# Optimization experiments

Measured on AMD Instinct MI355X. Metric: run time of the kernel, lower is better.

## Reference

```python
import jax, jax.numpy as jnp
import numpy as np

B, N, T, D = 4, 128, 64, 768
L_ATTN, HEADS = 4, 8
M_SSM = 4
D_INNER, D_STATE, HEADDIM = 1536, 64, 64
NHEADS = D_INNER // HEADDIM  # 24
D_CONV = 4
CONV_DIM = D_INNER + 2 * D_STATE  # 1664
IN_PROJ = 2 * D_INNER + 2 * D_STATE + NHEADS  # 3224
FFN_MULT = 4


def rmsnorm(x, w, eps=1e-5):
    return x * jax.lax.rsqrt(jnp.mean(x * x, -1, keepdims=True) + eps) * w


def mha(q_in, kv_in, Wq, Wk, Wv, Wo):
    b, lq, d = q_in.shape
    lk = kv_in.shape[1]
    dh = d // HEADS
    scale = 1.0 / float(np.sqrt(dh))
    q = (q_in @ Wq).reshape(b, lq, HEADS, dh)
    k = (kv_in @ Wk).reshape(b, lk, HEADS, dh)
    v = (kv_in @ Wv).reshape(b, lk, HEADS, dh)
    scores = jnp.einsum('bqhd,bkhd->bhqk', q, k) * scale
    attn = jax.nn.softmax(scores, axis=-1)
    o = jnp.einsum('bhqk,bkhd->bqhd', attn, v).reshape(b, lq, d)
    return o @ Wo


def mamba_block(x, in_proj_w, conv_w, conv_b, dt_bias, A_log, D_skip, norm_w, out_proj_w):
    # x: (b, l, D); selective-scan (Mamba2) with scalar-per-head A, ngroups=1
    b, l, _ = x.shape
    zxbcdt = x @ in_proj_w                       # (b, l, IN_PROJ)
    z = zxbcdt[..., :D_INNER]
    xBC = zxbcdt[..., D_INNER:D_INNER + CONV_DIM]
    dt = zxbcdt[..., D_INNER + CONV_DIM:]        # (b, l, NHEADS)
    # causal depthwise conv1d, kernel D_CONV
    xp = jnp.pad(xBC, ((0, 0), (D_CONV - 1, 0), (0, 0)))
    xc = sum(conv_w[k] * xp[:, k:k + l] for k in range(D_CONV)) + conv_b
    xc = jax.nn.silu(xc)
    xs = xc[..., :D_INNER].reshape(b, l, NHEADS, HEADDIM)
    Bm = xc[..., D_INNER:D_INNER + D_STATE]      # (b, l, D_STATE)
    Cm = xc[..., D_INNER + D_STATE:]             # (b, l, D_STATE)
    dt = jax.nn.softplus(dt + dt_bias)           # (b, l, NHEADS)
    A = -jnp.exp(A_log)                          # (NHEADS,)
    h0 = jnp.zeros((b, NHEADS, HEADDIM, D_STATE), x.dtype)

    def step(h, inp):
        xt, Bt, Ct, dtt = inp                    # (b,nh,hd), (b,ds), (b,ds), (b,nh)
        dA = jnp.exp(dtt * A)                    # (b, nh)
        h = h * dA[:, :, None, None] + (dtt[:, :, None, None] * xt[..., None]) * Bt[:, None, None, :]
        y = jnp.einsum('bhps,bs->bhp', h, Ct)
        return h, y

    hT, ys = jax.lax.scan(step, h0, (xs.transpose(1, 0, 2, 3), Bm.transpose(1, 0, 2), Cm.transpose(1, 0, 2), dt.transpose(1, 0, 2)))
    y = ys.transpose(1, 0, 2, 3) + D_skip[:, None] * xs  # skip connection per head
    y = y.reshape(b, l, D_INNER)
    y = rmsnorm(y * jax.nn.silu(z), norm_w)      # gated RMSNorm
    return y @ out_proj_w, hT


def reference(precepts, actions, attn_norm1_w, Wq, Wk, Wv, Wo, attn_norm2_w, ffn_w1, ffn_b1, ffn_w2, ffn_b2, ssm_norm_w, in_proj_w, conv_w, conv_b, dt_bias, A_log, D_skip, mamba_norm_w, out_proj_w, proj_w, proj_b):
    p = precepts.reshape(B * N, T, D)
    a = actions.reshape(B * N, T, D)
    for i in range(L_ATTN):
        cross = (i + 1) % 2 == 0
        q = rmsnorm(p, attn_norm1_w[i])
        kv = a if cross else q
        p = p + mha(q, kv, Wq[i], Wk[i], Wv[i], Wo[i])
        h_ = rmsnorm(p, attn_norm2_w[i])
        p = p + (jax.nn.gelu(h_ @ ffn_w1[i] + ffn_b1[i]) @ ffn_w2[i] + ffn_b2[i])
    # (b n) t d -> (b t) n d : scan over the num_steps axis
    z = p.reshape(B, N, T, D).transpose(0, 2, 1, 3).reshape(B * T, N, D)
    h_last = None
    for m in range(M_SSM):
        out, h_last = mamba_block(rmsnorm(z, ssm_norm_w[m]), in_proj_w[m], conv_w[m], conv_b[m], dt_bias[m], A_log[m], D_skip[m], mamba_norm_w[m], out_proj_w[m])
        z = z + out
    y = z @ proj_w + proj_b
    y = y.reshape(B, T, N, D).transpose(0, 2, 1, 3)  # b n t d
    return y, h_last


def setup_inputs() -> dict:
    key = jax.random.key(0)
    ks = jax.random.split(key, 16)
    s = 0.02
    f32 = jnp.float32
    return {
        'precepts': jax.random.normal(ks[0], (B, N, T, D), f32),
        'actions': jax.random.normal(ks[1], (B, N, T, D), f32),
        'attn_norm1_w': jnp.ones((L_ATTN, D), f32),
        'Wq': s * jax.random.normal(ks[2], (L_ATTN, D, D), f32),
        'Wk': s * jax.random.normal(ks[3], (L_ATTN, D, D), f32),
        'Wv': s * jax.random.normal(ks[4], (L_ATTN, D, D), f32),
        'Wo': s * jax.random.normal(ks[5], (L_ATTN, D, D), f32),
        'attn_norm2_w': jnp.ones((L_ATTN, D), f32),
        'ffn_w1': s * jax.random.normal(ks[6], (L_ATTN, D, FFN_MULT * D), f32),
        'ffn_b1': jnp.zeros((L_ATTN, FFN_MULT * D), f32),
        'ffn_w2': s * jax.random.normal(ks[7], (L_ATTN, FFN_MULT * D, D), f32),
        'ffn_b2': jnp.zeros((L_ATTN, D), f32),
        'ssm_norm_w': jnp.ones((M_SSM, D), f32),
        'in_proj_w': s * jax.random.normal(ks[8], (M_SSM, D, IN_PROJ), f32),
        'conv_w': s * jax.random.normal(ks[9], (M_SSM, D_CONV, CONV_DIM), f32),
        'conv_b': jnp.zeros((M_SSM, CONV_DIM), f32),
        'dt_bias': jax.random.uniform(ks[10], (M_SSM, NHEADS), f32, -2.0, 0.0),
        'A_log': jnp.broadcast_to(jnp.log(jnp.arange(1, NHEADS + 1, dtype=f32)), (M_SSM, NHEADS)),
        'D_skip': jnp.ones((M_SSM, NHEADS), f32),
        'mamba_norm_w': jnp.ones((M_SSM, D_INNER), f32),
        'out_proj_w': s * jax.random.normal(ks[11], (M_SSM, D_INNER, D), f32),
        'proj_w': s * jax.random.normal(ks[12], (D, D), f32),
        'proj_b': jnp.zeros((D,), f32),
    }
```

## Files before the change

kernel.cpp:

```cpp
#include <hip/hip_runtime.h>
#include <hip/hip_bf16.h>
#include <math.h>

constexpr long TOK  = 32768;
constexpr long HALF = TOK * 768;
constexpr int FLAG_ACC = 1, FLAG_GELU = 2, FLAG_PERM = 4, FLAG_BF16 = 8;

typedef __bf16 bf16x8 __attribute__((ext_vector_type(8)));
typedef __bf16 bf16x4 __attribute__((ext_vector_type(4)));
typedef float  f32x4  __attribute__((ext_vector_type(4)));

__device__ __forceinline__ void gload_lds16(const void* g, void* l) {
    __builtin_amdgcn_global_load_lds(
        (const __attribute__((address_space(1))) void*)g,
        (__attribute__((address_space(3))) void*)l, 16, 0, 0);
}
__device__ __forceinline__ float bf2f(__hip_bfloat16 v) { return __bfloat162float(v); }

__global__ __launch_bounds__(512, 2) void gemm256(
    const __hip_bfloat16* __restrict__ A,
    const __hip_bfloat16* __restrict__ BT,
    const float* __restrict__ bias,
    void* __restrict__ Cv, int ldc,
    int M, int N, int K, int flags, int moff)
{
    __shared__ __align__(16) __hip_bfloat16 As[2][256 * 64];
    __shared__ __align__(16) __hip_bfloat16 Bs[2][256 * 64];
    const int tid = threadIdx.x;
    const int wid = tid >> 6, lane = tid & 63;
    const int wm = wid >> 2, wn = wid & 3;
    const int lrow = lane & 15, lk = lane >> 4;
    const int nwg = gridDim.x * gridDim.y;
    const int orig = blockIdx.y * gridDim.x + blockIdx.x;
    const int q8 = nwg >> 3, r8 = nwg & 7;
    const int xcd = orig & 7, off = orig >> 3;
    const int wgid = (xcd < r8 ? xcd * (q8 + 1) : r8 * (q8 + 1) + (xcd - r8) * q8) + off;
    const int bm = (wgid / gridDim.x) * 256, bn = (wgid % gridDim.x) * 256;
    const int nk = K >> 6;

    f32x4 acc[4][8];
#pragma unroll
    for (int nf = 0; nf < 4; nf++)
#pragma unroll
        for (int mf = 0; mf < 8; mf++) acc[nf][mf] = f32x4{0.f, 0.f, 0.f, 0.f};

    bf16x8 Af[4][2];
    bf16x8 B0[2][2];
    bf16x8 B1[2][2];

    auto stage = [&](int kt, int which) {
        if (kt >= nk) return;
        const int dbuf = kt & 1;
        __hip_bfloat16* lbase = (which >= 2 ? &Bs[dbuf][0] : &As[dbuf][0]) + (which & 1) * 8192;
        const __hip_bfloat16* g = (which >= 2 ? BT : A);
        const int trow = (which >= 2 ? bn : bm) + (which & 1) * 128;
#pragma unroll
        for (int i = 0; i < 2; i++) {
            const int slot = i * 512 + tid;
            const int rl = slot >> 3, ch = slot & 7;
            const int sc = (ch ^ (rl & 7)) * 8;
            const long src = (long)(trow + rl) * K + (long)kt * 64 + sc;
            char* l = (char*)lbase + (i * 512 + wid * 64) * 16;
            gload_lds16(g + src, l);
        }
    };
    auto readA = [&](int dbuf, int mh) {
#pragma unroll
        for (int mq = 0; mq < 4; mq++)
#pragma unroll
            for (int ks = 0; ks < 2; ks++) {
                const int r = wm * 128 + mh * 64 + mq * 16 + lrow;
                const int ch = ((ks * 4 + lk) ^ (r & 7)) * 8;
                Af[mq][ks] = *(const bf16x8*)(const void*)&As[dbuf][r * 64 + ch];
            }
    };
    auto readB0 = [&](int dbuf) {
#pragma unroll
        for (int nf = 0; nf < 2; nf++)
#pragma unroll
            for (int ks = 0; ks < 2; ks++) {
                const int r = wn * 64 + nf * 16 + lrow;
                const int ch = ((ks * 4 + lk) ^ (r & 7)) * 8;
                B0[nf][ks] = *(const bf16x8*)(const void*)&Bs[dbuf][r * 64 + ch];
            }
    };
    auto readB1 = [&](int dbuf) {
#pragma unroll
        for (int nf = 0; nf < 2; nf++)
#pragma unroll
            for (int ks = 0; ks < 2; ks++) {
                const int r = wn * 64 + (2 + nf) * 16 + lrow;
                const int ch = ((ks * 4 + lk) ^ (r & 7)) * 8;
                B1[nf][ks] = *(const bf16x8*)(const void*)&Bs[dbuf][r * 64 + ch];
            }
    };

    stage(0, 0); stage(0, 1); stage(0, 2); stage(0, 3);
    stage(1, 2); stage(1, 3);
    asm volatile("s_waitcnt vmcnt(4)" ::: "memory");
    __builtin_amdgcn_s_barrier();

    for (int kt = 0; kt < nk; kt++) {
        const int cur = kt & 1;
        readA(cur, 0); readB0(cur);
        stage(kt + 1, 0); stage(kt + 1, 1);
        __builtin_amdgcn_s_barrier();
        __builtin_amdgcn_s_setprio(1);
#pragma unroll
        for (int ks = 0; ks < 2; ks++)
#pragma unroll
            for (int nf = 0; nf < 2; nf++)
#pragma unroll
                for (int mq = 0; mq < 4; mq++)
                    acc[nf][mq] = __builtin_amdgcn_mfma_f32_16x16x32_bf16(B0[nf][ks], Af[mq][ks], acc[nf][mq], 0, 0, 0);
        __builtin_amdgcn_s_setprio(0);
        __builtin_amdgcn_s_barrier();
        readB1(cur);
        __builtin_amdgcn_s_barrier();
        __builtin_amdgcn_s_setprio(1);
#pragma unroll
        for (int ks = 0; ks < 2; ks++)
#pragma unroll
            for (int nf = 0; nf < 2; nf++)
#pragma unroll
                for (int mq = 0; mq < 4; mq++)
                    acc[2 + nf][mq] = __builtin_amdgcn_mfma_f32_16x16x32_bf16(B1[nf][ks], Af[mq][ks], acc[2 + nf][mq], 0, 0, 0);
        __builtin_amdgcn_s_setprio(0);
        __builtin_amdgcn_s_barrier();
        readA(cur, 1);
        stage(kt + 2, 2);
        __builtin_amdgcn_s_barrier();
        __builtin_amdgcn_s_setprio(1);
#pragma unroll
        for (int ks = 0; ks < 2; ks++)
#pragma unroll
            for (int nf = 0; nf < 2; nf++)
#pragma unroll
                for (int mq = 0; mq < 4; mq++)
                    acc[2 + nf][4 + mq] = __builtin_amdgcn_mfma_f32_16x16x32_bf16(B1[nf][ks], Af[mq][ks], acc[2 + nf][4 + mq], 0, 0, 0);
        __builtin_amdgcn_s_setprio(0);
        __builtin_amdgcn_s_barrier();
        stage(kt + 2, 3);
        if (kt + 2 < nk) asm volatile("s_waitcnt vmcnt(4)" ::: "memory");
        else             asm volatile("s_waitcnt vmcnt(0)" ::: "memory");
        __builtin_amdgcn_s_barrier();
        __builtin_amdgcn_s_setprio(1);
#pragma unroll
        for (int ks = 0; ks < 2; ks++)
#pragma unroll
            for (int nf = 0; nf < 2; nf++)
#pragma unroll
                for (int mq = 0; mq < 4; mq++)
                    acc[nf][4 + mq] = __builtin_amdgcn_mfma_f32_16x16x32_bf16(B0[nf][ks], Af[mq][ks], acc[nf][4 + mq], 0, 0, 0);
        __builtin_amdgcn_s_setprio(0);
        __builtin_amdgcn_s_barrier();
    }

    float* Cf = (float*)Cv;
    __hip_bfloat16* Cb = (__hip_bfloat16*)Cv;
    if (flags & FLAG_BF16) {
        char* lw = (char*)&As[0][0] + (size_t)wid * (64 * 176);
        const int colg = bn + wn * 64;
#pragma unroll
        for (int half = 0; half < 2; half++) {
#pragma unroll
            for (int nf = 0; nf < 4; nf++) {
                const int col = nf * 16 + lk * 4;
                f32x4 b4 = f32x4{0.f, 0.f, 0.f, 0.f};
                if (bias) b4 = *(const f32x4*)&bias[colg + col];
#pragma unroll
                for (int m4 = 0; m4 < 4; m4++) {
                    const int row = m4 * 16 + lrow;
                    f32x4 v = acc[nf][half * 4 + m4] + b4;
                    if (flags & FLAG_GELU) {
#pragma unroll
                        for (int j = 0; j < 4; j++) {
                            const float x = v[j];
                            const float u = 1.5957691216057308f * (x + 0.044715f * x * x * x);
                            v[j] = x / (1.f + __expf(-u));
                        }
                    }
                    bf16x4 o;
                    o[0] = (__bf16)v[0]; o[1] = (__bf16)v[1];
                    o[2] = (__bf16)v[2]; o[3] = (__bf16)v[3];
                    *(bf16x4*)(void*)(lw + row * 176 + col * 2) = o;
                }
            }
            asm volatile("s_waitcnt lgkmcnt(0)" ::: "memory");
#pragma unroll
            for (int rr = 0; rr < 8; rr++) {
                const int row = rr * 8 + (lane >> 3);
                const long gr = (long)(bm + wm * 128 + half * 64 + row);
                const bf16x8 d = *(const bf16x8*)(const void*)(lw + row * 176 + (lane & 7) * 16);
                *(bf16x8*)(void*)&Cb[gr * ldc + colg + (lane & 7) * 8] = d;
            }
            asm volatile("s_waitcnt lgkmcnt(0)" ::: "memory");
        }
    } else {
#pragma unroll
        for (int nf = 0; nf < 4; nf++) {
            const int gcb = bn + wn * 64 + nf * 16 + lk * 4;
            if (gcb >= N) continue;
            f32x4 b4 = f32x4{0.f, 0.f, 0.f, 0.f};
            if (bias) b4 = *(const f32x4*)&bias[gcb];
#pragma unroll
            for (int mf = 0; mf < 8; mf++) {
                const int gr = bm + wm * 128 + mf * 16 + lrow;
                f32x4 v = acc[nf][mf] + b4;
                if (flags & FLAG_GELU) {
#pragma unroll
                    for (int j = 0; j < 4; j++) {
                        const float x = v[j];
                        const float u = 1.5957691216057308f * (x + 0.044715f * x * x * x);
                        v[j] = x / (1.f + __expf(-u));
                    }
                }
                if (flags & FLAG_PERM) {
                    const int mg = moff + gr;
                    const int b_ = mg >> 13, t_ = (mg >> 7) & 63, n_ = mg & 127;
                    *(f32x4*)&Cf[(((long)(b_ * 128 + n_)) * 64 + t_) * ldc + gcb] = v;
                } else if (flags & FLAG_ACC) {
                    float* dst = &Cf[(long)gr * ldc + gcb];
                    f32x4 old = *(const f32x4*)dst;
                    *(f32x4*)dst = old + v;
                } else {
                    *(f32x4*)&Cf[(long)gr * ldc + gcb] = v;
                }
            }
        }
    }
}

__global__ __launch_bounds__(256) void gemm_bf16(
    const __hip_bfloat16* __restrict__ A,
    const __hip_bfloat16* __restrict__ BT,
    const float* __restrict__ bias,
    void* __restrict__ Cv, int ldc,
    int M, int N, int K, int flags, int moff)
{
    __shared__ __hip_bfloat16 As[2][128 * 32];
    __shared__ __hip_bfloat16 Bs[2][128 * 32];
    const int tid = threadIdx.x;
    const int wv = tid >> 6, lane = tid & 63;
    const int nwg = gridDim.x * gridDim.y;
    const int orig = blockIdx.y * gridDim.x + blockIdx.x;
    const int q8 = nwg >> 3, r8 = nwg & 7;
    const int xcd = orig & 7, off = orig >> 3;
    const int wgid = (xcd < r8 ? xcd * (q8 + 1) : r8 * (q8 + 1) + (xcd - r8) * q8) + off;
    const int bm = (wgid / gridDim.x) * 128, bn = (wgid % gridDim.x) * 128;
    const int wr = (wv >> 1) * 64, wc = (wv & 1) * 64;
    const int lrow = lane & 15, lk = lane >> 4;
    const int ck = (lk ^ (lrow & 3) ^ ((lrow >> 2) & 3)) * 8;

    f32x4 acc[4][4];
#pragma unroll
    for (int n = 0; n < 4; n++)
#pragma unroll
        for (int m = 0; m < 4; m++) acc[n][m] = f32x4{0.f, 0.f, 0.f, 0.f};

    const int nk = K >> 5;
    auto stage = [&](int kt, int buf) {
#pragma unroll
        for (int i = 0; i < 2; i++) {
            const int lin = i * 256 + tid;
            const int row = lin >> 2;
            const int ks  = (((lin & 3) ^ (row & 3) ^ ((row >> 2) & 3)) * 8);
            const long asrc = (long)(bm + row) * K + kt * 32 + ks;
            const long bsrc = (long)(bn + row) * K + kt * 32 + ks;
            char* la = (char*)&As[buf][0] + (i * 256 + wv * 64) * 16;
            char* lb = (char*)&Bs[buf][0] + (i * 256 + wv * 64) * 16;
            gload_lds16(A + asrc, la);
            gload_lds16(BT + bsrc, lb);
        }
    };

    stage(0, 0);
    __syncthreads();
    for (int kt = 0; kt < nk; kt++) {
        const int cur = kt & 1;
        if (kt + 1 < nk) stage(kt + 1, cur ^ 1);
        bf16x8 af[4], bfr[4];
#pragma unroll
        for (int m = 0; m < 4; m++) {
            af[m]  = *(const bf16x8*)(const void*)&As[cur][(wr + m * 16 + lrow) * 32 + ck];
            bfr[m] = *(const bf16x8*)(const void*)&Bs[cur][(wc + m * 16 + lrow) * 32 + ck];
        }
#pragma unroll
        for (int n = 0; n < 4; n++)
#pragma unroll
            for (int m = 0; m < 4; m++)
                acc[n][m] = __builtin_amdgcn_mfma_f32_16x16x32_bf16(bfr[n], af[m], acc[n][m], 0, 0, 0);
        __syncthreads();
    }

    float* Cf = (float*)Cv;
    __hip_bfloat16* Cb = (__hip_bfloat16*)Cv;
#pragma unroll
    for (int n = 0; n < 4; n++) {
        const int gcb = bn + wc + n * 16 + lk * 4;
        if (gcb >= N) continue;
        f32x4 b4 = f32x4{0.f, 0.f, 0.f, 0.f};
        if (bias) b4 = *(const f32x4*)&bias[gcb];
#pragma unroll
        for (int m = 0; m < 4; m++) {
            const int gr = bm + wr + m * 16 + lrow;
            f32x4 v = acc[n][m] + b4;
            if (flags & FLAG_GELU) {
#pragma unroll
                for (int j = 0; j < 4; j++) {
                    const float x = v[j];
                    const float u = 1.5957691216057308f * (x + 0.044715f * x * x * x);
                    v[j] = x / (1.f + __expf(-u));
                }
            }
            if (flags & FLAG_PERM) {
                const int mg = moff + gr;
                const int b_ = mg >> 13, t_ = (mg >> 7) & 63, n_ = mg & 127;
                *(f32x4*)&Cf[(((long)(b_ * 128 + n_)) * 64 + t_) * ldc + gcb] = v;
            } else if (flags & FLAG_BF16) {
                __hip_bfloat16 o0 = __float2bfloat16(v[0]), o1 = __float2bfloat16(v[1]);
                __hip_bfloat16 o2 = __float2bfloat16(v[2]), o3 = __float2bfloat16(v[3]);
                ushort4 o = { *(ushort*)&o0, *(ushort*)&o1, *(ushort*)&o2, *(ushort*)&o3 };
                *(ushort4*)&Cb[(long)gr * ldc + gcb] = o;
            } else if (flags & FLAG_ACC) {
                float* dst = &Cf[(long)gr * ldc + gcb];
                f32x4 old = *(const f32x4*)dst;
                *(f32x4*)dst = old + v;
            } else {
                *(f32x4*)&Cf[(long)gr * ldc + gcb] = v;
            }
        }
    }
}

__global__ void convT_kernel(const float* __restrict__ W, __hip_bfloat16* __restrict__ WT,
                             int K, int N, int Npad)
{
    __shared__ float t[32][33];
    const int k0 = blockIdx.y * 32, n0 = blockIdx.x * 32;
    const int tx = threadIdx.x & 31, ty = threadIdx.x >> 5;
#pragma unroll
    for (int i = 0; i < 4; i++) {
        int k = k0 + ty + i * 8, n = n0 + tx;
        t[ty + i * 8][tx] = (k < K && n < N) ? W[(long)k * N + n] : 0.f;
    }
    __syncthreads();
#pragma unroll
    for (int i = 0; i < 4; i++) {
        int n = n0 + ty + i * 8, k = k0 + tx;
        if (n < Npad && k < K) WT[(long)n * K + k] = __float2bfloat16(t[tx][ty + i * 8]);
    }
}

__global__ void cvt_kernel(const float4* __restrict__ x, ushort4* __restrict__ y, long n4)
{
    long i = (long)blockIdx.x * 256 + threadIdx.x;
    if (i >= n4) return;
    float4 v = x[i];
    __hip_bfloat16 a = __float2bfloat16(v.x), b = __float2bfloat16(v.y);
    __hip_bfloat16 c = __float2bfloat16(v.z), d = __float2bfloat16(v.w);
    ushort4 o = { *(ushort*)&a, *(ushort*)&b, *(ushort*)&c, *(ushort*)&d };
    y[i] = o;
}

__global__ void rmsnorm_f32(const float* __restrict__ x, const float* __restrict__ w,
                            __hip_bfloat16* __restrict__ out, int D, int xs, int os, long nrows)
{
    const int wv = threadIdx.x >> 6, lane = threadIdx.x & 63;
    const long row = (long)blockIdx.x * 4 + wv;
    if (row >= nrows) return;
    const float* xr = x + row * xs;
    const int it = D >> 8;
    float ss = 0.f;
    for (int i = 0; i < it; i++) {
        const float4 v = *(const float4*)&xr[(i * 64 + lane) * 4];
        ss += v.x * v.x + v.y * v.y + v.z * v.z + v.w * v.w;
    }
    for (int o = 32; o; o >>= 1) ss += __shfl_xor(ss, o);
    const float sc = rsqrtf(ss / D + 1e-5f);
    __hip_bfloat16* orow = out + row * os;
    for (int i = 0; i < it; i++) {
        const int e = (i * 64 + lane) * 4;
        const float4 v = *(const float4*)&xr[e];
        const float4 g = *(const float4*)&w[e];
        bf16x4 o;
        o[0] = (__bf16)(v.x * sc * g.x); o[1] = (__bf16)(v.y * sc * g.y);
        o[2] = (__bf16)(v.z * sc * g.z); o[3] = (__bf16)(v.w * sc * g.w);
        *(bf16x4*)(void*)&orow[e] = o;
    }
}
__global__ void rmsnorm_b16(const __hip_bfloat16* __restrict__ x, const float* __restrict__ w,
                            __hip_bfloat16* __restrict__ out, int D, int xs, int os, long nrows)
{
    const int wv = threadIdx.x >> 6, lane = threadIdx.x & 63;
    const long row = (long)blockIdx.x * 4 + wv;
    if (row >= nrows) return;
    const __hip_bfloat16* xr = x + row * xs;
    const int it = D >> 8;
    float ss = 0.f;
    for (int i = 0; i < it; i++) {
        const bf16x4 v = *(const bf16x4*)(const void*)&xr[(i * 64 + lane) * 4];
#pragma unroll
        for (int e = 0; e < 4; e++) { const float f = (float)v[e]; ss += f * f; }
    }
    for (int o = 32; o; o >>= 1) ss += __shfl_xor(ss, o);
    const float sc = rsqrtf(ss / D + 1e-5f);
    __hip_bfloat16* orow = out + row * os;
    for (int i = 0; i < it; i++) {
        const int e = (i * 64 + lane) * 4;
        const bf16x4 v = *(const bf16x4*)(const void*)&xr[e];
        const float4 g = *(const float4*)&w[e];
        bf16x4 o;
        o[0] = (__bf16)((float)v[0] * sc * g.x); o[1] = (__bf16)((float)v[1] * sc * g.y);
        o[2] = (__bf16)((float)v[2] * sc * g.z); o[3] = (__bf16)((float)v[3] * sc * g.w);
        *(bf16x4*)(void*)&orow[e] = o;
    }
}

__global__ __launch_bounds__(256) void attn_kernel(
    const __hip_bfloat16* __restrict__ QKV, __hip_bfloat16* __restrict__ O)
{
    __shared__ __align__(16) __hip_bfloat16 Qs[3 * 64 * 32];
    __shared__ __align__(16) __hip_bfloat16 Ks[3 * 64 * 32];
    __shared__ __align__(16) __hip_bfloat16 VT[2 * 96 * 32];
    __shared__ __align__(16) __hip_bfloat16 Ps[2 * 64 * 32];
    const int tid = threadIdx.x;
    const int wid = tid >> 6, lane = tid & 63;
    const int lrow = lane & 15, lk = lane >> 4;
    const int b = blockIdx.x >> 3, h = blockIdx.x & 7;
    const long base = (long)b * 64 * 2304 + h * 96;

#pragma unroll
    for (int i = 0; i < 3; i++) {
        const int v = i * 256 + tid;
        const int r = v / 12, c8 = v - r * 12;
        const int kst = c8 >> 2, ch = c8 & 3, slot = ch ^ (r & 3);
        const bf16x8 q = *(const bf16x8*)(const void*)&QKV[base + (long)r * 2304 + c8 * 8];
        const bf16x8 k = *(const bf16x8*)(const void*)&QKV[base + (long)r * 2304 + 768 + c8 * 8];
        *(bf16x8*)(void*)&Qs[(kst * 64 + r) * 32 + slot * 8] = q;
        *(bf16x8*)(void*)&Ks[(kst * 64 + r) * 32 + slot * 8] = k;
    }
    for (int i = 0; i < 16; i++) {
        const int k = wid * 16 + i;
        const __hip_bfloat16* vrow = &QKV[base + (long)k * 2304 + 1536];
        const int sb = (k >> 3) & 3, khi = k >> 5, klo = k & 7;
        {
            const int d = lane;
            VT[(khi * 96 + d) * 32 + ((sb ^ (d & 3)) * 8) + klo] = vrow[d];
        }
        if (lane < 32) {
            const int d = 64 + lane;
            VT[(khi * 96 + d) * 32 + ((sb ^ (d & 3)) * 8) + klo] = vrow[d];
        }
    }
    __syncthreads();

    const int ck = (lk ^ (lrow & 3)) * 8;
    f32x4 s[4];
#pragma unroll
    for (int n = 0; n < 4; n++) s[n] = f32x4{0.f, 0.f, 0.f, 0.f};
#pragma unroll
    for (int kst = 0; kst < 3; kst++) {
        const bf16x8 qf = *(const bf16x8*)(const void*)&Qs[(kst * 64 + wid * 16 + lrow) * 32 + ck];
#pragma unroll
        for (int n = 0; n < 4; n++) {
            const bf16x8 kf = *(const bf16x8*)(const void*)&Ks[(kst * 64 + n * 16 + lrow) * 32 + ck];
            s[n] = __builtin_amdgcn_mfma_f32_16x16x32_bf16(qf, kf, s[n], 0, 0, 0);
        }
    }
    const float scale = 0.102062072615966f;
#pragma unroll
    for (int n = 0; n < 4; n++) s[n] *= scale;
    float inv[4];
#pragma unroll
    for (int j = 0; j < 4; j++) {
        float mx = fmaxf(fmaxf(s[0][j], s[1][j]), fmaxf(s[2][j], s[3][j]));
        mx = fmaxf(mx, __shfl_xor(mx, 1));
        mx = fmaxf(mx, __shfl_xor(mx, 2));
        mx = fmaxf(mx, __shfl_xor(mx, 4));
        mx = fmaxf(mx, __shfl_xor(mx, 8));
        float sum = 0.f;
#pragma unroll
        for (int n = 0; n < 4; n++) { s[n][j] = __expf(s[n][j] - mx); sum += s[n][j]; }
        sum += __shfl_xor(sum, 1);
        sum += __shfl_xor(sum, 2);
        sum += __shfl_xor(sum, 4);
        sum += __shfl_xor(sum, 8);
        inv[j] = 1.f / sum;
    }
#pragma unroll
    for (int n = 0; n < 4; n++) {
        const int k = n * 16 + lrow;
        const int kst = n >> 1, kc = ((n & 1) << 1) + (lrow >> 3), ke = lrow & 7;
#pragma unroll
        for (int j = 0; j < 4; j++) {
            const int q = wid * 16 + lk * 4 + j;
            Ps[(kst * 64 + q) * 32 + ((kc ^ (q & 3)) * 8) + ke] = __float2bfloat16(s[n][j] * inv[j]);
        }
    }
    __syncthreads();

    const int wq = wid >> 1, wd = wid & 1;
    f32x4 y[3][2];
#pragma unroll
    for (int mv = 0; mv < 3; mv++)
#pragma unroll
        for (int np = 0; np < 2; np++) y[mv][np] = f32x4{0.f, 0.f, 0.f, 0.f};
#pragma unroll
    for (int ks = 0; ks < 2; ks++) {
        bf16x8 vf[3], pf[2];
#pragma unroll
        for (int mv = 0; mv < 3; mv++)
            vf[mv] = *(const bf16x8*)(const void*)&VT[(ks * 96 + wd * 48 + mv * 16 + lrow) * 32 + ck];
#pragma unroll
        for (int np = 0; np < 2; np++)
            pf[np] = *(const bf16x8*)(const void*)&Ps[(ks * 64 + wq * 32 + np * 16 + lrow) * 32 + ck];
#pragma unroll
        for (int mv = 0; mv < 3; mv++)
#pragma unroll
            for (int np = 0; np < 2; np++)
                y[mv][np] = __builtin_amdgcn_mfma_f32_16x16x32_bf16(vf[mv], pf[np], y[mv][np], 0, 0, 0);
    }
#pragma unroll
    for (int mv = 0; mv < 3; mv++) {
        const int d0 = wd * 48 + mv * 16 + lk * 4;
#pragma unroll
        for (int np = 0; np < 2; np++) {
            const int q = wq * 32 + np * 16 + lrow;
            bf16x4 o;
#pragma unroll
            for (int j = 0; j < 4; j++) o[j] = (__bf16)y[mv][np][j];
            *(bf16x4*)(void*)&O[(long)(b * 64 + q) * 768 + h * 96 + d0] = o;
        }
    }
}

__global__ void transpose_kernel(const float* __restrict__ P, float* __restrict__ Z)
{
    long lin = (long)blockIdx.x * 256 + threadIdx.x;
    if (lin >= HALF) return;
    int d = (int)(lin % 768);
    long rowz = lin / 768;
    int n = rowz & 127, t = (int)((rowz >> 7) & 63), b = (int)(rowz >> 13);
    long rowp = ((long)(b * 128 + n)) * 64 + t;
    Z[lin] = P[rowp * 768 + d];
}

__global__ __launch_bounds__(256) void conv_kernel(
    const __hip_bfloat16* __restrict__ zx, const float* __restrict__ cw,
    const float* __restrict__ cb, __hip_bfloat16* __restrict__ xc,
    __hip_bfloat16* __restrict__ bcB, long rows)
{
    const long r = blockIdx.x;
    const int tid = threadIdx.x;
    if (tid >= 208) return;
    const int c0 = tid * 8;
    const int n = (int)(r & 127);
    float acc[8];
    {
        const float4 b0 = *(const float4*)&cb[c0];
        const float4 b1 = *(const float4*)&cb[c0 + 4];
        acc[0] = b0.x; acc[1] = b0.y; acc[2] = b0.z; acc[3] = b0.w;
        acc[4] = b1.x; acc[5] = b1.y; acc[6] = b1.z; acc[7] = b1.w;
    }
#pragma unroll
    for (int k = 0; k < 4; k++) {
        if (n - 3 + k < 0) continue;
        const bf16x8 xv = *(const bf16x8*)(const void*)&zx[(r - 3 + k) * 3328 + 1536 + c0];
        const float4 w0 = *(const float4*)&cw[k * 1664 + c0];
        const float4 w1 = *(const float4*)&cw[k * 1664 + c0 + 4];
        acc[0] += w0.x * (float)xv[0]; acc[1] += w0.y * (float)xv[1];
        acc[2] += w0.z * (float)xv[2]; acc[3] += w0.w * (float)xv[3];
        acc[4] += w1.x * (float)xv[4]; acc[5] += w1.y * (float)xv[5];
        acc[6] += w1.z * (float)xv[6]; acc[7] += w1.w * (float)xv[7];
    }
    bf16x8 o;
#pragma unroll
    for (int e = 0; e < 8; e++) {
        const float s = acc[e] / (1.f + __expf(-acc[e]));
        o[e] = (__bf16)s;
    }
    if (c0 < 1536) *(bf16x8*)(void*)&xc[r * 1664 + c0] = o;
    else           *(bf16x8*)(void*)&bcB[r * 128 + (c0 - 1536)] = o;
}

__global__ void dt_kernel(const __hip_bfloat16* __restrict__ zx, const float* __restrict__ bias,
                          float* __restrict__ dtf, long count)
{
    long lin = (long)blockIdx.x * 256 + threadIdx.x;
    if (lin >= count) return;
    int h = (int)(lin % 24);
    long r = lin / 24;
    float v = bf2f(zx[r * 3328 + 3200 + h]) + bias[h];
    dtf[lin] = (v > 0.f) ? v + log1pf(expf(-v)) : log1pf(expf(v));
}

__global__ __launch_bounds__(256) void ssd_kernel(
    const __hip_bfloat16* __restrict__ zx0, const float* __restrict__ dtf0,
    const __hip_bfloat16* __restrict__ bcB0, __hip_bfloat16* __restrict__ xc0,
    const float* __restrict__ Alog, const float* __restrict__ Dskip,
    float* __restrict__ hout, int bt0)
{
    __shared__ __align__(16) char SM[50688];
    __hip_bfloat16* Cl  = (__hip_bfloat16*)SM;
    __hip_bfloat16* Bl  = Cl + 8192;
    __hip_bfloat16* Ml  = (__hip_bfloat16*)SM;
    __hip_bfloat16* XTl = (__hip_bfloat16*)(SM + 32768);
    __hip_bfloat16* BTl = (__hip_bfloat16*)SM;
    float* cum = (float*)(SM + 49152);
    float* dtl = cum + 128;
    float* wl  = dtl + 128;

    const int tid = threadIdx.x;
    const int wid = tid >> 6, lane = tid & 63;
    const int lrow = lane & 15, lk = lane >> 4;
    const int btl = blockIdx.x / 24, h = blockIdx.x % 24;
    const long rowbase = (long)btl * 128;

    const __hip_bfloat16* zxp = zx0 + rowbase * 3328 + h * 64;
    const float* dtp = dtf0 + rowbase * 24;
    const __hip_bfloat16* bcp = bcB0 + rowbase * 128;
    __hip_bfloat16* xcp = xc0 + rowbase * 1664 + h * 64;

    const float A  = -__expf(Alog[h]);
    const float Dh = Dskip[h];

#pragma unroll
    for (int i = 0; i < 4; i++) {
        const int v = tid + i * 256;
        const int row = v >> 3, c8 = v & 7;
        const int kst = c8 >> 2, ch = c8 & 3;
        const int slot = ch ^ (row & 3);
        bf16x8 vB = *(const bf16x8*)(const void*)&bcp[(long)row * 128 + c8 * 8];
        bf16x8 vC = *(const bf16x8*)(const void*)&bcp[(long)row * 128 + 64 + c8 * 8];
        *(bf16x8*)(void*)&Bl[(kst * 128 + row) * 32 + slot * 8] = vB;
        *(bf16x8*)(void*)&Cl[(kst * 128 + row) * 32 + slot * 8] = vC;
    }
    for (int i = 0; i < 32; i++) {
        const int t = wid * 32 + i;
        const int slot = (i >> 3) ^ (lane & 3);
        XTl[(wid * 64 + lane) * 32 + slot * 8 + (i & 7)] = xcp[(long)t * 1664 + lane];
    }
    if (wid == 0) {
        const float d0 = dtp[(long)(2 * lane) * 24 + h];
        const float d1 = dtp[(long)(2 * lane + 1) * 24 + h];
        const float a0 = d0 * A, a1v = d1 * A;
        float sc = a0 + a1v;
#pragma unroll
        for (int o = 1; o < 64; o <<= 1) {
            const float pv = __shfl_up(sc, o);
            if (lane >= o) sc += pv;
        }
        const float tot = __shfl(sc, 63);
        cum[2 * lane]     = sc - a1v;
        cum[2 * lane + 1] = sc;
        dtl[2 * lane]     = d0;
        dtl[2 * lane + 1] = d1;
        wl[2 * lane]      = __expf(tot - (sc - a1v)) * d0;
        wl[2 * lane + 1]  = __expf(tot - sc) * d1;
    }
    __syncthreads();

    const int wr1 = (wid >> 1) * 64, wc1 = (wid & 1) * 64;
    const int ck = (lk ^ (lrow & 3)) * 8;
    f32x4 a1[4][4];
#pragma unroll
    for (int m = 0; m < 4; m++)
#pragma unroll
        for (int n = 0; n < 4; n++) a1[m][n] = f32x4{0.f, 0.f, 0.f, 0.f};
#pragma unroll
    for (int kst = 0; kst < 2; kst++) {
        bf16x8 ca[4], bb[4];
#pragma unroll
        for (int m = 0; m < 4; m++)
            ca[m] = *(const bf16x8*)(const void*)&Cl[(kst * 128 + wr1 + m * 16 + lrow) * 32 + ck];
#pragma unroll
        for (int n = 0; n < 4; n++)
            bb[n] = *(const bf16x8*)(const void*)&Bl[(kst * 128 + wc1 + n * 16 + lrow) * 32 + ck];
#pragma unroll
        for (int m = 0; m < 4; m++)
#pragma unroll
            for (int n = 0; n < 4; n++)
                a1[m][n] = __builtin_amdgcn_mfma_f32_16x16x32_bf16(bb[n], ca[m], a1[m][n], 0, 0, 0);
    }
    __syncthreads();

#pragma unroll
    for (int m = 0; m < 4; m++) {
        const int t = wr1 + m * 16 + lrow;
        const float ct = cum[t];
        const int trow32 = ((t >> 5) * 128 + t) * 32;
        const int txor = (t & 3);
#pragma unroll
        for (int n = 0; n < 4; n++) {
            const int j0 = wc1 + n * 16 + lk * 4;
            const f32x4 cj = *(const f32x4*)&cum[j0];
            const f32x4 dj = *(const f32x4*)&dtl[j0];
            bf16x4 o;
#pragma unroll
            for (int jj = 0; jj < 4; jj++) {
                const int j = j0 + jj;
                float val = 0.f;
                if (j <= t) val = a1[m][n][jj] * __expf(ct - cj[jj]) * dj[jj];
                o[jj] = (__bf16)val;
            }
            const int jst = j0 >> 5, jc = (j0 >> 3) & 3, je = j0 & 7;
            *(bf16x4*)(void*)&Ml[(jst * 128 + t) * 32 + ((jc ^ txor) * 8) + je] = o;
        }
    }
    __syncthreads();

    const int wr2 = (wid >> 1) * 64, wc2 = (wid & 1) * 32;
    f32x4 a2[4][2];
#pragma unroll
    for (int m = 0; m < 4; m++)
#pragma unroll
        for (int n = 0; n < 2; n++) a2[m][n] = f32x4{0.f, 0.f, 0.f, 0.f};
#pragma unroll
    for (int kst = 0; kst < 4; kst++) {
        bf16x8 am[4], bn[2];
#pragma unroll
        for (int m = 0; m < 4; m++)
            am[m] = *(const bf16x8*)(const void*)&Ml[(kst * 128 + wr2 + m * 16 + lrow) * 32 + ck];
#pragma unroll
        for (int n = 0; n < 2; n++)
            bn[n] = *(const bf16x8*)(const void*)&XTl[(kst * 64 + wc2 + n * 16 + lrow) * 32 + ck];
#pragma unroll
        for (int m = 0; m < 4; m++)
#pragma unroll
            for (int n = 0; n < 2; n++)
                a2[m][n] = __builtin_amdgcn_mfma_f32_16x16x32_bf16(bn[n], am[m], a2[m][n], 0, 0, 0);
    }

#pragma unroll
    for (int m = 0; m < 4; m++) {
        const int t = wr2 + m * 16 + lrow;
#pragma unroll
        for (int n = 0; n < 2; n++) {
            const int p0 = wc2 + n * 16 + lk * 4;
            const bf16x4 x4 = *(const bf16x4*)(const void*)&xcp[(long)t * 1664 + p0];
            const bf16x4 z4 = *(const bf16x4*)(const void*)&zxp[(long)t * 3328 + p0];
            bf16x4 o;
#pragma unroll
            for (int jj = 0; jj < 4; jj++) {
                const float x = (float)x4[jj];
                const float zg = (float)z4[jj];
                const float y = (a2[m][n][jj] + Dh * x) * (zg / (1.f + __expf(-zg)));
                o[jj] = (__bf16)y;
            }
            *(bf16x4*)(void*)&xcp[(long)t * 1664 + p0] = o;
        }
    }

    if (hout) {
        __syncthreads();
        for (int i = 0; i < 32; i++) {
            const int j = wid * 32 + i;
            const int slot = (i >> 3) ^ (lane & 3);
            BTl[(wid * 64 + lane) * 32 + slot * 8 + (j & 7)] = bcp[(long)j * 128 + lane];
        }
        __syncthreads();
        const int wrp = (wid >> 1) * 32, wcs = (wid & 1) * 32;
        f32x4 a3[2][2];
#pragma unroll
        for (int m = 0; m < 2; m++)
#pragma unroll
            for (int n = 0; n < 2; n++) a3[m][n] = f32x4{0.f, 0.f, 0.f, 0.f};
#pragma unroll
        for (int kst = 0; kst < 4; kst++) {
            const int jb = kst * 32 + lk * 8;
            const f32x4 wa = *(const f32x4*)&wl[jb];
            const f32x4 wb = *(const f32x4*)&wl[jb + 4];
            bf16x8 xw[2], bn[2];
#pragma unroll
            for (int m = 0; m < 2; m++) {
                bf16x8 xr = *(const bf16x8*)(const void*)&XTl[(kst * 64 + wrp + m * 16 + lrow) * 32 + ck];
                bf16x8 t;
#pragma unroll
                for (int e = 0; e < 4; e++) t[e] = (__bf16)((float)xr[e] * wa[e]);
#pragma unroll
                for (int e = 0; e < 4; e++) t[4 + e] = (__bf16)((float)xr[4 + e] * wb[e]);
                xw[m] = t;
            }
#pragma unroll
            for (int n = 0; n < 2; n++)
                bn[n] = *(const bf16x8*)(const void*)&BTl[(kst * 64 + wcs + n * 16 + lrow) * 32 + ck];
#pragma unroll
            for (int m = 0; m < 2; m++)
#pragma unroll
                for (int n = 0; n < 2; n++)
                    a3[m][n] = __builtin_amdgcn_mfma_f32_16x16x32_bf16(xw[m], bn[n], a3[m][n], 0, 0, 0);
        }
        float* hp = hout + ((long)(bt0 + btl) * 24 + h) * 4096;
#pragma unroll
        for (int m = 0; m < 2; m++) {
            const int pb = wrp + m * 16 + lk * 4;
#pragma unroll
            for (int n = 0; n < 2; n++) {
                const int s = wcs + n * 16 + lrow;
#pragma unroll
                for (int jj = 0; jj < 4; jj++)
                    hp[(long)(pb + jj) * 64 + s] = a3[m][n][jj];
            }
        }
    }
}

extern "C" void kernel_launch(void* const* d_in, const int* in_sizes, int n_in,
                              void* d_out, int out_size, void* d_ws, size_t ws_size,
                              hipStream_t stream)
{
    const float* precepts  = (const float*)d_in[0];
    const float* actions   = (const float*)d_in[1];
    const float* attn_n1   = (const float*)d_in[2];
    const float* Wq        = (const float*)d_in[3];
    const float* Wk        = (const float*)d_in[4];
    const float* Wv        = (const float*)d_in[5];
    const float* Wo        = (const float*)d_in[6];
    const float* attn_n2   = (const float*)d_in[7];
    const float* ffn_w1    = (const float*)d_in[8];
    const float* ffn_b1    = (const float*)d_in[9];
    const float* ffn_w2    = (const float*)d_in[10];
    const float* ffn_b2    = (const float*)d_in[11];
    const float* ssm_norm  = (const float*)d_in[12];
    const float* in_proj   = (const float*)d_in[13];
    const float* conv_w    = (const float*)d_in[14];
    const float* conv_b    = (const float*)d_in[15];
    const float* dt_bias   = (const float*)d_in[16];
    const float* A_log     = (const float*)d_in[17];
    const float* D_skip    = (const float*)d_in[18];
    const float* mamba_nw  = (const float*)d_in[19];
    const float* out_proj  = (const float*)d_in[20];
    const float* proj_w    = (const float*)d_in[21];
    const float* proj_b    = (const float*)d_in[22];

    float* out  = (float*)d_out;
    float* Z    = out;
    float* P    = out + HALF;
    float* hout = out + HALF;

    __hip_bfloat16* wb = (__hip_bfloat16*)d_ws;
    long wo = 0;
    auto walloc = [&](long els) { __hip_bfloat16* p = wb + wo; wo += els; return p; };
    __hip_bfloat16* WqkvT = walloc(4L * 2304 * 768);
    __hip_bfloat16* W1T   = walloc(4L * 3072 * 768);
    __hip_bfloat16* W2T   = walloc(4L * 768 * 3072);
    __hip_bfloat16* inT   = walloc(4L * 3328 * 768);
    __hip_bfloat16* outT  = walloc(4L * 768 * 1536);
    __hip_bfloat16* projT = walloc(768L * 768);
    __hip_bfloat16* WoT   = walloc(4L * 768 * 768);
    char* pbase = (char*)(wb + ((wo + 255) & ~255L));
    const size_t used_w = (size_t)(pbase - (char*)d_ws);
    const size_t avail = ws_size > used_w ? ws_size - used_w : 0;

    int CB = 512;
    while (CB > 8 && (unsigned long long)CB * 884736ull > avail) CB >>= 1;
    int CBT = 256;
    while (CBT > 2 && (unsigned long long)CBT * 1912832ull > avail) CBT >>= 1;

    auto gemm = [&](const __hip_bfloat16* A, const __hip_bfloat16* BT, const float* bias,
                    void* C, int ldc, int M, int N, int Npad, int K, int flags, int moff) {
        if ((M & 255) == 0 && (Npad & 255) == 0 && (K & 63) == 0) {
            dim3 g(Npad / 256, M / 256);
            hipLaunchKernelGGL(gemm256, g, dim3(512), 0, stream,
                               A, BT, bias, C, ldc, M, N, K, flags, moff);
        } else {
            dim3 g(Npad / 128, M / 128);
            hipLaunchKernelGGL(gemm_bf16, g, dim3(256), 0, stream,
                               A, BT, bias, C, ldc, M, N, K, flags, moff);
        }
    };
    auto cvtT = [&](const float* W, __hip_bfloat16* WT, int K, int N, int Npad) {
        dim3 g((Npad + 31) / 32, (K + 31) / 32);
        hipLaunchKernelGGL(convT_kernel, g, dim3(256), 0, stream, W, WT, K, N, Npad);
    };
    auto cvt = [&](const float* x, __hip_bfloat16* y, long n) {
        long n4 = n / 4;
        hipLaunchKernelGGL(cvt_kernel, dim3((n4 + 255) / 256), dim3(256), 0, stream,
                           (const float4*)x, (ushort4*)y, n4);
    };
    auto rmsF = [&](const float* x, const float* w, __hip_bfloat16* o, int D, int xs, int os, long rows) {
        hipLaunchKernelGGL(rmsnorm_f32, dim3((rows + 3) / 4), dim3(256), 0, stream,
                           x, w, o, D, xs, os, rows);
    };
    auto rmsB = [&](const __hip_bfloat16* x, const float* w, __hip_bfloat16* o, int D, int xs, int os, long rows) {
        hipLaunchKernelGGL(rmsnorm_b16, dim3((rows + 3) / 4), dim3(256), 0, stream,
                           x, w, o, D, xs, os, rows);
    };

    for (int l = 0; l < 4; l++) {
        cvtT(Wq + (long)l * 589824, WqkvT + (long)l * 2304 * 768,                768, 768, 768);
        cvtT(Wk + (long)l * 589824, WqkvT + (long)l * 2304 * 768 +  768L * 768,  768, 768, 768);
        cvtT(Wv + (long)l * 589824, WqkvT + (long)l * 2304 * 768 + 1536L * 768,  768, 768, 768);
        cvtT(Wo + (long)l * 589824, WoT + (long)l * 589824, 768, 768, 768);
        cvtT(ffn_w1 + (long)l * 2359296, W1T + (long)l * 2359296, 768, 3072, 3072);
        cvtT(ffn_w2 + (long)l * 2359296, W2T + (long)l * 2359296, 3072, 768, 768);
    }
    for (int m = 0; m < 4; m++) {
        cvtT(in_proj + (long)m * 768 * 3224, inT + (long)m * 3328 * 768, 768, 3224, 3328);
        cvtT(out_proj + (long)m * 1536 * 768, outT + (long)m * 768 * 1536, 1536, 768, 768);
    }
    cvtT(proj_w, projT, 768, 768, 768);

    hipMemcpyAsync(P, precepts, HALF * sizeof(float), hipMemcpyDeviceToDevice, stream);
    {
        const long rA = (long)CB * 64;
        __hip_bfloat16* bufA   = (__hip_bfloat16*)pbase;
        __hip_bfloat16* actB   = bufA + rA * 768;
        __hip_bfloat16* bufQKV = actB + rA * 768;
        __hip_bfloat16* bufH   = bufQKV + rA * 2304;
        const int nac = 512 / CB;
        const int Mr = (int)rA;
        if (nac == 1) cvt(actions, actB, rA * 768);
        for (int layer = 0; layer < 4; layer++) {
            const bool cross = ((layer + 1) % 2) == 0;
            for (int c = 0; c < nac; c++) {
                const long tok0 = (long)c * rA;
                float* Pc = P + tok0 * 768;
                rmsF(Pc, attn_n1 + layer * 768, bufA, 768, 768, 768, Mr);
                if (!cross) {
                    gemm(bufA, WqkvT + (long)layer * 2304 * 768, nullptr, bufQKV, 2304,
                         Mr, 2304, 2304, 768, FLAG_BF16, 0);
                } else {
                    if (nac != 1) cvt(actions + tok0 * 768, actB, rA * 768);
                    gemm(bufA, WqkvT + (long)layer * 2304 * 768, nullptr, bufQKV, 2304,
                         Mr, 768, 768, 768, FLAG_BF16, 0);
                    gemm(actB, WqkvT + (long)layer * 2304 * 768 + 768L * 768, nullptr,
                         bufQKV + 768, 2304, Mr, 1536, 1536, 768, FLAG_BF16, 0);
                }
                hipLaunchKernelGGL(attn_kernel, dim3(CB * 8), dim3(256), 0, stream,
                                   bufQKV, bufA);
                gemm(bufA, WoT + (long)layer * 589824, nullptr, Pc, 768,
                     Mr, 768, 768, 768, FLAG_ACC, 0);
                rmsF(Pc, attn_n2 + layer * 768, bufA, 768, 768, 768, Mr);
                gemm(bufA, W1T + (long)layer * 2359296, ffn_b1 + layer * 3072, bufH, 3072,
                     Mr, 3072, 3072, 768, FLAG_GELU | FLAG_BF16, 0);
                gemm(bufH, W2T + (long)layer * 2359296, ffn_b2 + layer * 768, Pc, 768,
                     Mr, 768, 768, 3072, FLAG_ACC, 0);
            }
        }
    }

    hipLaunchKernelGGL(transpose_kernel, dim3((int)((HALF + 255) / 256)), dim3(256), 0, stream, P, Z);

    {
        const long rM = (long)CBT * 128;
        __hip_bfloat16* xn  = (__hip_bfloat16*)pbase;
        __hip_bfloat16* zx  = xn + rM * 768;
        float*          dtf = (float*)(zx + rM * 3328);
        __hip_bfloat16* xc  = (__hip_bfloat16*)(dtf + rM * 24);
        __hip_bfloat16* yb  = xc + rM * 1664;
        __hip_bfloat16* bcB = yb + rM * 1536;
        const int nmc = 256 / CBT;
        const int Mr = (int)rM;
        for (int m = 0; m < 4; m++) {
            for (int c = 0; c < nmc; c++) {
                float* Zc = Z + (long)c * rM * 768;
                rmsF(Zc, ssm_norm + m * 768, xn, 768, 768, 768, Mr);
                gemm(xn, inT + (long)m * 3328 * 768, nullptr, zx, 3328,
                     Mr, 3224, 3328, 768, FLAG_BF16, 0);
                hipLaunchKernelGGL(conv_kernel, dim3((int)rM), dim3(256), 0, stream,
                                   zx, conv_w + m * 4 * 1664, conv_b + m * 1664, xc, bcB, rM);
                const long dtn = rM * 24;
                hipLaunchKernelGGL(dt_kernel, dim3((int)((dtn + 255) / 256)), dim3(256), 0, stream,
                                   zx, dt_bias + m * 24, dtf, dtn);
                hipLaunchKernelGGL(ssd_kernel, dim3(CBT * 24), dim3(256), 0, stream,
                                   zx, dtf, bcB, xc, A_log + m * 24, D_skip + m * 24,
                                   (m == 3) ? hout : nullptr, c * CBT);
                rmsB(xc, mamba_nw + m * 1536, yb, 1536, 1664, 1536, Mr);
                gemm(yb, outT + (long)m * 768 * 1536, nullptr, Zc, 768,
                     Mr, 768, 768, 1536, FLAG_ACC, 0);
            }
        }
    }

    {
        __hip_bfloat16* Zb = (__hip_bfloat16*)pbase;
        cvt(Z, Zb, HALF);
        gemm(Zb, projT, proj_b, out, 768, 32768, 768, 768, 768, FLAG_PERM, 0);
    }
}
```

Before: 6.231 ms.

## Keep residual streams in bf16 with fused bf16 accumulate epilogue

Stores the attention and SSM residual streams (P, Z) in bf16 instead of fp32, with the GEMM epilogues gaining a bf16 read-add-write path for FLAG_ACC. This halves residual memory traffic in rmsnorm, the accumulate GEMMs and the transpose, and it drops the final fp32-to-bf16 conversion before the projection GEMM. In exchange the residual is accumulated at bf16 precision across 8 layers, which adds rounding error that may fail accuracy tolerances.

```diff
diff --git a/kernel.cpp b/kernel.cpp
--- a/kernel.cpp
+++ b/kernel.cpp
@@ -179,6 +179,12 @@
                             const float u = 1.5957691216057308f * (x + 0.044715f * x * x * x);
                             v[j] = x / (1.f + __expf(-u));
                         }
+                    }
+                    if (flags & FLAG_ACC) {
+                        const long gr = (long)(bm + wm * 128 + half * 64 + row);
+                        const bf16x4 old = *(const bf16x4*)(const void*)&Cb[gr * ldc + colg + col];
+#pragma unroll
+                        for (int j = 0; j < 4; j++) v[j] += (float)old[j];
                     }
                     bf16x4 o;
                     o[0] = (__bf16)v[0]; o[1] = (__bf16)v[1];
@@ -318,6 +324,11 @@
                 const int b_ = mg >> 13, t_ = (mg >> 7) & 63, n_ = mg & 127;
                 *(f32x4*)&Cf[(((long)(b_ * 128 + n_)) * 64 + t_) * ldc + gcb] = v;
             } else if (flags & FLAG_BF16) {
+                if (flags & FLAG_ACC) {
+                    const bf16x4 old = *(const bf16x4*)(const void*)&Cb[(long)gr * ldc + gcb];
+#pragma unroll
+                    for (int j = 0; j < 4; j++) v[j] += (float)old[j];
+                }
                 __hip_bfloat16 o0 = __float2bfloat16(v[0]), o1 = __float2bfloat16(v[1]);
                 __hip_bfloat16 o2 = __float2bfloat16(v[2]), o3 = __float2bfloat16(v[3]);
                 ushort4 o = { *(ushort*)&o0, *(ushort*)&o1, *(ushort*)&o2, *(ushort*)&o3 };
@@ -363,32 +374,6 @@
     y[i] = o;
 }
 
-__global__ void rmsnorm_f32(const float* __restrict__ x, const float* __restrict__ w,
-                            __hip_bfloat16* __restrict__ out, int D, int xs, int os, long nrows)
-{
-    const int wv = threadIdx.x >> 6, lane = threadIdx.x & 63;
-    const long row = (long)blockIdx.x * 4 + wv;
-    if (row >= nrows) return;
-    const float* xr = x + row * xs;
-    const int it = D >> 8;
-    float ss = 0.f;
-    for (int i = 0; i < it; i++) {
-        const float4 v = *(const float4*)&xr[(i * 64 + lane) * 4];
-        ss += v.x * v.x + v.y * v.y + v.z * v.z + v.w * v.w;
-    }
-    for (int o = 32; o; o >>= 1) ss += __shfl_xor(ss, o);
-    const float sc = rsqrtf(ss / D + 1e-5f);
-    __hip_bfloat16* orow = out + row * os;
-    for (int i = 0; i < it; i++) {
-        const int e = (i * 64 + lane) * 4;
-        const float4 v = *(const float4*)&xr[e];
-        const float4 g = *(const float4*)&w[e];
-        bf16x4 o;
-        o[0] = (__bf16)(v.x * sc * g.x); o[1] = (__bf16)(v.y * sc * g.y);
-        o[2] = (__bf16)(v.z * sc * g.z); o[3] = (__bf16)(v.w * sc * g.w);
-        *(bf16x4*)(void*)&orow[e] = o;
-    }
-}
 __global__ void rmsnorm_b16(const __hip_bfloat16* __restrict__ x, const float* __restrict__ w,
                             __hip_bfloat16* __restrict__ out, int D, int xs, int os, long nrows)
 {
@@ -535,15 +520,16 @@
     }
 }
 
-__global__ void transpose_kernel(const float* __restrict__ P, float* __restrict__ Z)
-{
-    long lin = (long)blockIdx.x * 256 + threadIdx.x;
-    if (lin >= HALF) return;
-    int d = (int)(lin % 768);
-    long rowz = lin / 768;
+__global__ void transpose_kernel(const __hip_bfloat16* __restrict__ P, __hip_bfloat16* __restrict__ Z)
+{
+    long lin4 = (long)blockIdx.x * 256 + threadIdx.x;
+    if (lin4 >= HALF / 4) return;
+    int d4 = (int)(lin4 % 192);
+    long rowz = lin4 / 192;
     int n = rowz & 127, t = (int)((rowz >> 7) & 63), b = (int)(rowz >> 13);
     long rowp = ((long)(b * 128 + n)) * 64 + t;
-    Z[lin] = P[rowp * 768 + d];
+    const bf16x4 v = *(const bf16x4*)(const void*)&P[rowp * 768 + d4 * 4];
+    *(bf16x4*)(void*)&Z[rowz * 768 + d4 * 4] = v;
 }
 
 __global__ __launch_bounds__(256) void conv_kernel(
@@ -689,7 +675,6 @@
     for (int m = 0; m < 4; m++) {
         const int t = wr1 + m * 16 + lrow;
         const float ct = cum[t];
-        const int trow32 = ((t >> 5) * 128 + t) * 32;
         const int txor = (t & 3);
 #pragma unroll
         for (int n = 0; n < 4; n++) {
@@ -835,8 +820,7 @@
     const float* proj_b    = (const float*)d_in[22];
 
     float* out  = (float*)d_out;
-    float* Z    = out;
-    float* P    = out + HALF;
+    __hip_bfloat16* Pb = (__hip_bfloat16*)(out + HALF);
     float* hout = out + HALF;
 
     __hip_bfloat16* wb = (__hip_bfloat16*)d_ws;
@@ -849,6 +833,7 @@
     __hip_bfloat16* outT  = walloc(4L * 768 * 1536);
     __hip_bfloat16* projT = walloc(768L * 768);
     __hip_bfloat16* WoT   = walloc(4L * 768 * 768);
+    __hip_bfloat16* Zb    = walloc(TOK * 768);
     char* pbase = (char*)(wb + ((wo + 255) & ~255L));
     const size_t used_w = (size_t)(pbase - (char*)d_ws);
     const size_t avail = ws_size > used_w ? ws_size - used_w : 0;
@@ -879,10 +864,6 @@
         hipLaunchKernelGGL(cvt_kernel, dim3((n4 + 255) / 256), dim3(256), 0, stream,
                            (const float4*)x, (ushort4*)y, n4);
     };
-    auto rmsF = [&](const float* x, const float* w, __hip_bfloat16* o, int D, int xs, int os, long rows) {
-        hipLaunchKernelGGL(rmsnorm_f32, dim3((rows + 3) / 4), dim3(256), 0, stream,
-                           x, w, o, D, xs, os, rows);
-    };
     auto rmsB = [&](const __hip_bfloat16* x, const float* w, __hip_bfloat16* o, int D, int xs, int os, long rows) {
         hipLaunchKernelGGL(rmsnorm_b16, dim3((rows + 3) / 4), dim3(256), 0, stream,
                            x, w, o, D, xs, os, rows);
@@ -902,7 +883,7 @@
     }
     cvtT(proj_w, projT, 768, 768, 768);
 
-    hipMemcpyAsync(P, precepts, HALF * sizeof(float), hipMemcpyDeviceToDevice, stream);
+    cvt(precepts, Pb, HALF);
     {
         const long rA = (long)CB * 64;
         __hip_bfloat16* bufA   = (__hip_bfloat16*)pbase;
@@ -916,8 +897,8 @@
             const bool cross = ((layer + 1) % 2) == 0;
             for (int c = 0; c < nac; c++) {
                 const long tok0 = (long)c * rA;
-                float* Pc = P + tok0 * 768;
-                rmsF(Pc, attn_n1 + layer * 768, bufA, 768, 768, 768, Mr);
+                __hip_bfloat16* Pc = Pb + tok0 * 768;
+                rmsB(Pc, attn_n1 + layer * 768, bufA, 768, 768, 768, Mr);
                 if (!cross) {
                     gemm(bufA, WqkvT + (long)layer * 2304 * 768, nullptr, bufQKV, 2304,
                          Mr, 2304, 2304, 768, FLAG_BF16, 0);
@@ -931,17 +912,17 @@
                 hipLaunchKernelGGL(attn_kernel, dim3(CB * 8), dim3(256), 0, stream,
                                    bufQKV, bufA);
                 gemm(bufA, WoT + (long)layer * 589824, nullptr, Pc, 768,
-                     Mr, 768, 768, 768, FLAG_ACC, 0);
-                rmsF(Pc, attn_n2 + layer * 768, bufA, 768, 768, 768, Mr);
+                     Mr, 768, 768, 768, FLAG_ACC | FLAG_BF16, 0);
+                rmsB(Pc, attn_n2 + layer * 768, bufA, 768, 768, 768, Mr);
                 gemm(bufA, W1T + (long)layer * 2359296, ffn_b1 + layer * 3072, bufH, 3072,
                      Mr, 3072, 3072, 768, FLAG_GELU | FLAG_BF16, 0);
                 gemm(bufH, W2T + (long)layer * 2359296, ffn_b2 + layer * 768, Pc, 768,
-                     Mr, 768, 768, 3072, FLAG_ACC, 0);
-            }
-        }
-    }
-
-    hipLaunchKernelGGL(transpose_kernel, dim3((int)((HALF + 255) / 256)), dim3(256), 0, stream, P, Z);
+                     Mr, 768, 768, 3072, FLAG_ACC | FLAG_BF16, 0);
+            }
+        }
+    }
+
+    hipLaunchKernelGGL(transpose_kernel, dim3((int)((HALF / 4 + 255) / 256)), dim3(256), 0, stream, Pb, Zb);
 
     {
         const long rM = (long)CBT * 128;
@@ -955,8 +936,8 @@
         const int Mr = (int)rM;
         for (int m = 0; m < 4; m++) {
             for (int c = 0; c < nmc; c++) {
-                float* Zc = Z + (long)c * rM * 768;
-                rmsF(Zc, ssm_norm + m * 768, xn, 768, 768, 768, Mr);
+                __hip_bfloat16* Zc = Zb + (long)c * rM * 768;
+                rmsB(Zc, ssm_norm + m * 768, xn, 768, 768, 768, Mr);
                 gemm(xn, inT + (long)m * 3328 * 768, nullptr, zx, 3328,
                      Mr, 3224, 3328, 768, FLAG_BF16, 0);
                 hipLaunchKernelGGL(conv_kernel, dim3((int)rM), dim3(256), 0, stream,
@@ -969,14 +950,10 @@
                                    (m == 3) ? hout : nullptr, c * CBT);
                 rmsB(xc, mamba_nw + m * 1536, yb, 1536, 1664, 1536, Mr);
                 gemm(yb, outT + (long)m * 768 * 1536, nullptr, Zc, 768,
-                     Mr, 768, 768, 1536, FLAG_ACC, 0);
-            }
-        }
-    }
-
-    {
-        __hip_bfloat16* Zb = (__hip_bfloat16*)pbase;
-        cvt(Z, Zb, HALF);
-        gemm(Zb, projT, proj_b, out, 768, 32768, 768, 768, 768, FLAG_PERM, 0);
-    }
-}
+                     Mr, 768, 768, 1536, FLAG_ACC | FLAG_BF16, 0);
+            }
+        }
+    }
+
+    gemm(Zb, projT, proj_b, out, 768, 32768, 768, 768, 768, FLAG_PERM, 0);
+}
```

Measured after the change: 5.829 ms. -6.4%, faster.
